# Optimization experiments

Hardware: AMD Instinct MI355X
Metric: run time of the kernel (lower is better)

## Reference

```python
import jax, jax.numpy as jnp
import numpy as np

D = 33        # n_vertices
HID = 256     # hidden_features
N_RANKS = 5


def setup_inputs() -> dict:
    key = jax.random.key(0)
    ks = jax.random.split(key, 8)
    img = jax.random.uniform(ks[0], (1, 3, 2160, 3840), dtype=jnp.float32)
    param = jax.random.normal(ks[1], (1, N_RANKS), dtype=jnp.float32) * 0.1

    def lin(k, fan_in, fan_out):
        lim = 1.0 / np.sqrt(fan_in)
        kw, kb = jax.random.split(k)
        W = jax.random.uniform(kw, (fan_in, fan_out), minval=-lim, maxval=lim, dtype=jnp.float32)
        b = jax.random.uniform(kb, (fan_out,), minval=-lim, maxval=lim, dtype=jnp.float32)
        return W, b

    W0, b0 = lin(ks[2], 11, HID)
    W1, b1 = lin(ks[3], HID, HID)
    W2, b2 = lin(ks[4], HID, HID)
    W3, b3 = lin(ks[5], HID, HID)
    W4, b4 = lin(ks[6], HID, 3)
    return dict(img=img, param=param, W0=W0, b0=b0, W1=W1, b1=b1,
                W2=W2, b2=b2, W3=W3, b3=b3, W4=W4, b4=b4)


def _identity_lut_flat():
    # torch: stack(meshgrid(ij), 0)/ (D-1), flip(0), reshape (1,3,D^3)
    v = jnp.arange(D, dtype=jnp.float32)
    g = jnp.stack(jnp.meshgrid(v, v, v, indexing='ij'), axis=0) / (D - 1)
    return g[::-1].reshape(1, 3, -1)  # (1, 3, 35937)


def _nilut(intensity, W0, b0, W1, b1, W2, b2, W3, b3, W4, b4):
    # intensity: (B, N, 8) = [r, g, b, params...]
    inp = jnp.concatenate([intensity, jnp.sort(intensity[..., :3], axis=-1)], axis=-1)  # (B,N,11)
    zero_inp = inp[:1].at[:, :, 3:-3].set(0.0)  # zero the param channels

    def net(x):
        h = jax.nn.relu(x @ W0 + b0)
        h = jnp.tanh(h @ W1 + b1)
        h = jnp.tanh(h @ W2 + b2)
        h = jnp.tanh(h @ W3 + b3)
        return h @ W4 + b4

    return net(inp) - net(zero_inp) + intensity[..., :3]


def _trilinear_lookup(img, luts):
    # img: (B,3,H,W) in [0,1]; luts: (B,3,D,D,D) indexed [c, b_idx, g_idx, r_idx]
    s = img * (D - 1)
    idx = jnp.clip(jnp.floor(s), 0, D - 2).astype(jnp.int32)
    f = s - idx.astype(s.dtype)

    def one(lut_b, idx_b, f_b):
        ir, ig, ib = idx_b[0], idx_b[1], idx_b[2]
        fr, fg, fb = f_b[0], f_b[1], f_b[2]

        def g(db, dg, dr):
            return lut_b[:, ib + db, ig + dg, ir + dr]  # (3,H,W)

        return (g(0, 0, 0) * (1 - fb) * (1 - fg) * (1 - fr)
                + g(0, 0, 1) * (1 - fb) * (1 - fg) * fr
                + g(0, 1, 0) * (1 - fb) * fg * (1 - fr)
                + g(0, 1, 1) * (1 - fb) * fg * fr
                + g(1, 0, 0) * fb * (1 - fg) * (1 - fr)
                + g(1, 0, 1) * fb * (1 - fg) * fr
                + g(1, 1, 0) * fb * fg * (1 - fr)
                + g(1, 1, 1) * fb * fg * fr)

    return jax.vmap(one)(luts, idx, f)


def reference(img, param, W0, b0, W1, b1, W2, b2, W3, b3, W4, b4):
    B = param.shape[0]
    ident = _identity_lut_flat()                              # (1,3,N)
    Nl = ident.shape[2]
    tiled = jnp.broadcast_to(param[:, :, None], (B, N_RANKS, Nl))
    ins = jnp.concatenate([jnp.broadcast_to(ident, (B, 3, Nl)), tiled], axis=1)  # (B,8,N)
    ins = jnp.transpose(ins, (0, 2, 1))                       # (B,N,8)
    luts = _nilut(ins, W0, b0, W1, b1, W2, b2, W3, b3, W4, b4)  # (B,N,3)
    luts = jnp.transpose(luts, (0, 2, 1)).reshape(B, 3, D, D, D)
    img_rep = jnp.broadcast_to(img, (B,) + img.shape[1:])
    return _trilinear_lookup(img_rep, luts)
```

## Files before the change

### kernel.cpp

```cpp
#include <hip/hip_runtime.h>
#include <hip/hip_fp16.h>
#include <math.h>

#define NPTS 35937
#define HID 256
#define TPB 256

typedef __attribute__((ext_vector_type(8))) short short8;
typedef __attribute__((ext_vector_type(4))) float f32x4;

__device__ __forceinline__ float fast_tanh(float x) {
    float e = __expf(2.0f * x);
    return 1.0f - __fdividef(2.0f, e + 1.0f);
}

__device__ __forceinline__ short f2bf(float f) {
    union { float f; unsigned u; } v; v.f = f;
    unsigned r = (v.u + 0x7fffu + ((v.u >> 16) & 1u)) >> 16;
    return (short)r;
}

__device__ __forceinline__ unsigned cvt_pk_bf16(float a, float b) {
    unsigned r;
    asm("v_cvt_pk_bf16_f32 %0, %1, %2" : "=v"(r) : "v"(a), "v"(b));
    return r;
}

#define W1P_OFF 8192
#define W2P_OFF 73728
#define W3P_OFF 139264
#define W4P_OFF 204800
#define CELL_BYTE_OFF 992896

__global__ __launch_bounds__(256) void pack_weights_kernel(
    const float* __restrict__ W0, const float* __restrict__ W1,
    const float* __restrict__ W2, const float* __restrict__ W3,
    const float* __restrict__ W4, short* __restrict__ P)
{
    int id = blockIdx.x * 256 + threadIdx.x;
    if (id >= 26112) return;
    const float* W; int f, NT, KREAL, NROW; long pbase;
    if (id < 1024)       { W = W0; f = id;         NT = 16; KREAL = 11;  NROW = 256; pbase = 0; }
    else if (id < 9216)  { W = W1; f = id - 1024;  NT = 16; KREAL = 256; NROW = 256; pbase = W1P_OFF; }
    else if (id < 17408) { W = W2; f = id - 9216;  NT = 16; KREAL = 256; NROW = 256; pbase = W2P_OFF; }
    else if (id < 25600) { W = W3; f = id - 17408; NT = 16; KREAL = 256; NROW = 256; pbase = W3P_OFF; }
    else                 { W = W4; f = id - 25600; NT = 1;  KREAL = 256; NROW = 3;   pbase = W4P_OFF; }
    int lane = f & 63;
    int tile = f >> 6;
    int nt = tile % NT, kt = tile / NT;
    int n  = nt * 16 + (lane & 15);
    int k0 = kt * 32 + ((lane >> 4) & 3) * 8;
    short v[8];
    #pragma unroll
    for (int j = 0; j < 8; ++j) {
        int k = k0 + j;
        float x = (k < KREAL && n < NROW) ? W[k * NROW + n] : 0.0f;
        v[j] = f2bf(x);
    }
    *(short8*)(P + pbase + (long)f * 8) = *(short8*)v;
}

#define HSTR 264

__global__ __launch_bounds__(256) void nilut_mfma_kernel(
    const float* __restrict__ param, const short* __restrict__ P,
    const float* __restrict__ b0, const float* __restrict__ b1,
    const float* __restrict__ b2, const float* __restrict__ b3,
    const float* __restrict__ b4, __half* __restrict__ cells)
{
    __shared__ short Hs[32][HSTR];
    __shared__ short Is[32][40];
    __shared__ float OB[32][4];

    const int t = threadIdx.x;
    const int pblock = blockIdx.x * 16;
    const int lane = t & 63;
    const int wid  = t >> 6;
    const int lr = lane & 15;
    const int hi = lane >> 4;
    const int k8 = hi * 8;

    if (t < 32) {
        int pn = pblock + (t >> 1);
        if (pn >= NPTS) pn = NPTS - 1;
        int v = t & 1;
        int ii = pn / 1089;
        int rem = pn - ii * 1089;
        int jj = rem / 33;
        int kk = rem - jj * 33;
        float r = kk * (1.0f / 32.0f);
        float g = jj * (1.0f / 32.0f);
        float b = ii * (1.0f / 32.0f);
        float lo = fminf(r, fminf(g, b));
        float hv = fmaxf(r, fmaxf(g, b));
        float mid = r + g + b - lo - hv;
        Is[t][0] = f2bf(r); Is[t][1] = f2bf(g); Is[t][2] = f2bf(b);
        #pragma unroll
        for (int q = 0; q < 5; ++q)
            Is[t][3 + q] = (v == 0) ? f2bf(param[q]) : (short)0;
        Is[t][8] = f2bf(lo); Is[t][9] = f2bf(mid); Is[t][10] = f2bf(hv);
        #pragma unroll
        for (int q = 11; q < 40; ++q) Is[t][q] = (short)0;
    }
    __syncthreads();

    f32x4 acc[2][4];
    const int nbase = wid * 64 + hi * 4;

    {
        #pragma unroll
        for (int c = 0; c < 4; ++c) {
            float4 bv = *(const float4*)(b0 + nbase + c * 16);
            f32x4 in = {bv.x, bv.y, bv.z, bv.w};
            #pragma unroll
            for (int rt = 0; rt < 2; ++rt) acc[rt][c] = in;
        }
        short8 a[2], bfr[4];
        #pragma unroll
        for (int rt = 0; rt < 2; ++rt) a[rt] = *(const short8*)&Is[rt * 16 + lr][k8];
        #pragma unroll
        for (int c = 0; c < 4; ++c)
            bfr[c] = *(const short8*)(P + ((long)(wid * 4 + c) * 64 + lane) * 8);
        #pragma unroll
        for (int rt = 0; rt < 2; ++rt)
            #pragma unroll
            for (int c = 0; c < 4; ++c)
                acc[rt][c] = __builtin_amdgcn_mfma_f32_16x16x32_bf16(bfr[c], a[rt], acc[rt][c], 0, 0, 0);
        #pragma unroll
        for (int rt = 0; rt < 2; ++rt)
            #pragma unroll
            for (int c = 0; c < 4; ++c) {
                uint2 w;
                w.x = cvt_pk_bf16(fmaxf(acc[rt][c][0], 0.0f), fmaxf(acc[rt][c][1], 0.0f));
                w.y = cvt_pk_bf16(fmaxf(acc[rt][c][2], 0.0f), fmaxf(acc[rt][c][3], 0.0f));
                *(uint2*)&Hs[rt * 16 + lr][nbase + c * 16] = w;
            }
    }
    __syncthreads();

    const long loff[3] = {W1P_OFF, W2P_OFF, W3P_OFF};
    const float* bptr[3];
    bptr[0] = b1; bptr[1] = b2; bptr[2] = b3;
    for (int L = 0; L < 3; ++L) {
        const short* WL = P + loff[L];
        const float* bb = bptr[L];
        #pragma unroll
        for (int c = 0; c < 4; ++c) {
            float4 bv = *(const float4*)(bb + nbase + c * 16);
            f32x4 in = {bv.x, bv.y, bv.z, bv.w};
            #pragma unroll
            for (int rt = 0; rt < 2; ++rt) acc[rt][c] = in;
        }
        #pragma unroll
        for (int kt = 0; kt < 8; ++kt) {
            short8 a[2], bfr[4];
            #pragma unroll
            for (int rt = 0; rt < 2; ++rt)
                a[rt] = *(const short8*)&Hs[rt * 16 + lr][kt * 32 + k8];
            #pragma unroll
            for (int c = 0; c < 4; ++c)
                bfr[c] = *(const short8*)(WL + ((long)(kt * 16 + wid * 4 + c) * 64 + lane) * 8);
            #pragma unroll
            for (int rt = 0; rt < 2; ++rt)
                #pragma unroll
                for (int c = 0; c < 4; ++c)
                    acc[rt][c] = __builtin_amdgcn_mfma_f32_16x16x32_bf16(bfr[c], a[rt], acc[rt][c], 0, 0, 0);
        }
        __syncthreads();
        #pragma unroll
        for (int rt = 0; rt < 2; ++rt)
            #pragma unroll
            for (int c = 0; c < 4; ++c) {
                uint2 w;
                w.x = cvt_pk_bf16(fast_tanh(acc[rt][c][0]), fast_tanh(acc[rt][c][1]));
                w.y = cvt_pk_bf16(fast_tanh(acc[rt][c][2]), fast_tanh(acc[rt][c][3]));
                *(uint2*)&Hs[rt * 16 + lr][nbase + c * 16] = w;
            }
        __syncthreads();
    }

    if (wid < 2) {
        float bv = (lr < 3) ? b4[lr] : 0.0f;
        f32x4 a4 = {bv, bv, bv, bv};
        const short* WL = P + W4P_OFF;
        #pragma unroll
        for (int kt = 0; kt < 8; ++kt) {
            short8 a = *(const short8*)&Hs[wid * 16 + lr][kt * 32 + k8];
            short8 b = *(const short8*)(WL + ((long)kt * 64 + lane) * 8);
            a4 = __builtin_amdgcn_mfma_f32_16x16x32_bf16(a, b, a4, 0, 0, 0);
        }
        if (lr < 3) {
            #pragma unroll
            for (int q = 0; q < 4; ++q)
                OB[wid * 16 + hi * 4 + q][lr] = a4[q];
        }
    }
    __syncthreads();

    if (t < 16) {
        int n = pblock + t;
        if (n < NPTS) {
            int ii = n / 1089;
            int rem = n - ii * 1089;
            int jj = rem / 33;
            int kk = rem - jj * 33;
            float vr = OB[2 * t][0] - OB[2 * t + 1][0] + kk * (1.0f / 32.0f);
            float vg = OB[2 * t][1] - OB[2 * t + 1][1] + jj * (1.0f / 32.0f);
            float vb = OB[2 * t][2] - OB[2 * t + 1][2] + ii * (1.0f / 32.0f);
            union { __half h[4]; uint2 u; } pk;
            pk.h[0] = __float2half_rn(vr);
            pk.h[1] = __float2half_rn(vg);
            pk.h[2] = __float2half_rn(vb);
            pk.h[3] = __float2half_rn(0.0f);
            #pragma unroll
            for (int corner = 0; corner < 8; ++corner) {
                int dr = corner & 1, dg = (corner >> 1) & 1, db = corner >> 2;
                int cr = kk - dr, cg = jj - dg, cb = ii - db;
                if ((unsigned)cr < 32u && (unsigned)cg < 32u && (unsigned)cb < 32u) {
                    long cell = cb * 1024 + cg * 32 + cr;
                    *(uint2*)(cells + cell * 32 + corner * 4) = pk.u;
                }
            }
        }
    }
}

#define LERP(a, b, f) fmaf((f), (b) - (a), (a))

__global__ __launch_bounds__(256) void apply_lut_kernel(
    const float* __restrict__ img, const __half* __restrict__ cells,
    float* __restrict__ out)
{
    const int NP = 2160 * 3840;
    int idx = blockIdx.x * blockDim.x + threadIdx.x;
    int p = idx * 4;
    if (p >= NP) return;

    float4 rv = *(const float4*)(img + p);
    float4 gv = *(const float4*)(img + NP + p);
    float4 bv = *(const float4*)(img + 2 * NP + p);

    float rr[4] = {rv.x, rv.y, rv.z, rv.w};
    float gg[4] = {gv.x, gv.y, gv.z, gv.w};
    float bb[4] = {bv.x, bv.y, bv.z, bv.w};
    float ox[4], oy[4], oz[4];

    #pragma unroll
    for (int u = 0; u < 4; ++u) {
        float sr = rr[u] * 32.0f, sg = gg[u] * 32.0f, sb = bb[u] * 32.0f;
        float fir = fminf(fmaxf(floorf(sr), 0.0f), 31.0f);
        float fig = fminf(fmaxf(floorf(sg), 0.0f), 31.0f);
        float fib = fminf(fmaxf(floorf(sb), 0.0f), 31.0f);
        float fr = sr - fir, fg = sg - fig, fb = sb - fib;
        int ir = (int)fir, ig = (int)fig, ib = (int)fib;

        const short8* cb = (const short8*)(cells + ((long)(ib * 1024 + ig * 32 + ir)) * 32);
        union { short8 s; __half h[8]; } u0, u1, u2, u3;
        u0.s = cb[0]; u1.s = cb[1]; u2.s = cb[2]; u3.s = cb[3];

        float v00[3], v01[3], v10[3], v11[3];
        #pragma unroll
        for (int c = 0; c < 3; ++c) {
            v00[c] = LERP(__half2float(u0.h[c]), __half2float(u0.h[c + 4]), fr);
            v01[c] = LERP(__half2float(u1.h[c]), __half2float(u1.h[c + 4]), fr);
            v10[c] = LERP(__half2float(u2.h[c]), __half2float(u2.h[c + 4]), fr);
            v11[c] = LERP(__half2float(u3.h[c]), __half2float(u3.h[c + 4]), fr);
        }
        ox[u] = LERP(LERP(v00[0], v01[0], fg), LERP(v10[0], v11[0], fg), fb);
        oy[u] = LERP(LERP(v00[1], v01[1], fg), LERP(v10[1], v11[1], fg), fb);
        oz[u] = LERP(LERP(v00[2], v01[2], fg), LERP(v10[2], v11[2], fg), fb);
    }

    *(float4*)(out + p)          = make_float4(ox[0], ox[1], ox[2], ox[3]);
    *(float4*)(out + NP + p)     = make_float4(oy[0], oy[1], oy[2], oy[3]);
    *(float4*)(out + 2 * NP + p) = make_float4(oz[0], oz[1], oz[2], oz[3]);
}

extern "C" void kernel_launch(void* const* d_in, const int* in_sizes, int n_in,
                              void* d_out, int out_size, void* d_ws, size_t ws_size,
                              hipStream_t stream) {
    const float* img   = (const float*)d_in[0];
    const float* param = (const float*)d_in[1];
    const float* W0 = (const float*)d_in[2];
    const float* b0 = (const float*)d_in[3];
    const float* W1 = (const float*)d_in[4];
    const float* b1 = (const float*)d_in[5];
    const float* W2 = (const float*)d_in[6];
    const float* b2 = (const float*)d_in[7];
    const float* W3 = (const float*)d_in[8];
    const float* b3 = (const float*)d_in[9];
    const float* W4 = (const float*)d_in[10];
    const float* b4 = (const float*)d_in[11];

    short*  P     = (short*)d_ws;
    __half* cells = (__half*)((char*)d_ws + CELL_BYTE_OFF);
    float*  out   = (float*)d_out;

    hipLaunchKernelGGL(pack_weights_kernel, dim3(102), dim3(TPB), 0, stream,
                       W0, W1, W2, W3, W4, P);

    int lut_blocks = (NPTS + 15) / 16;
    hipLaunchKernelGGL(nilut_mfma_kernel, dim3(lut_blocks), dim3(TPB), 0, stream,
                       param, P, b0, b1, b2, b3, b4, cells);

    const int NP = 2160 * 3840;
    int apply_blocks = (NP / 4 + TPB - 1) / TPB;
    hipLaunchKernelGGL(apply_lut_kernel, dim3(apply_blocks), dim3(TPB), 0, stream,
                       img, cells, out);
}
```

Before: 132.6 us.

## Double-buffer image tiles into LDS via async global_load_lds in apply kernel

```diff
diff --git a/kernel.cpp b/kernel.cpp
--- a/kernel.cpp
+++ b/kernel.cpp
@@ -226,54 +226,84 @@
 }
 
 #define LERP(a, b, f) fmaf((f), (b) - (a), (a))
+#define NP_TOTAL (2160 * 3840)
+#define AP_BLOCKS 2025
+#define AP_TILES 4
 
 __global__ __launch_bounds__(256) void apply_lut_kernel(
     const float* __restrict__ img, const __half* __restrict__ cells,
     float* __restrict__ out)
 {
-    const int NP = 2160 * 3840;
-    int idx = blockIdx.x * blockDim.x + threadIdx.x;
-    int p = idx * 4;
-    if (p >= NP) return;
-
-    float4 rv = *(const float4*)(img + p);
-    float4 gv = *(const float4*)(img + NP + p);
-    float4 bv = *(const float4*)(img + 2 * NP + p);
-
-    float rr[4] = {rv.x, rv.y, rv.z, rv.w};
-    float gg[4] = {gv.x, gv.y, gv.z, gv.w};
-    float bb[4] = {bv.x, bv.y, bv.z, bv.w};
-    float ox[4], oy[4], oz[4];
-
-    #pragma unroll
-    for (int u = 0; u < 4; ++u) {
-        float sr = rr[u] * 32.0f, sg = gg[u] * 32.0f, sb = bb[u] * 32.0f;
-        float fir = fminf(fmaxf(floorf(sr), 0.0f), 31.0f);
-        float fig = fminf(fmaxf(floorf(sg), 0.0f), 31.0f);
-        float fib = fminf(fmaxf(floorf(sb), 0.0f), 31.0f);
-        float fr = sr - fir, fg = sg - fig, fb = sb - fib;
-        int ir = (int)fir, ig = (int)fig, ib = (int)fib;
-
-        const short8* cb = (const short8*)(cells + ((long)(ib * 1024 + ig * 32 + ir)) * 32);
-        union { short8 s; __half h[8]; } u0, u1, u2, u3;
-        u0.s = cb[0]; u1.s = cb[1]; u2.s = cb[2]; u3.s = cb[3];
-
-        float v00[3], v01[3], v10[3], v11[3];
-        #pragma unroll
-        for (int c = 0; c < 3; ++c) {
-            v00[c] = LERP(__half2float(u0.h[c]), __half2float(u0.h[c + 4]), fr);
-            v01[c] = LERP(__half2float(u1.h[c]), __half2float(u1.h[c + 4]), fr);
-            v10[c] = LERP(__half2float(u2.h[c]), __half2float(u2.h[c + 4]), fr);
-            v11[c] = LERP(__half2float(u3.h[c]), __half2float(u3.h[c + 4]), fr);
-        }
-        ox[u] = LERP(LERP(v00[0], v01[0], fg), LERP(v10[0], v11[0], fg), fb);
-        oy[u] = LERP(LERP(v00[1], v01[1], fg), LERP(v10[1], v11[1], fg), fb);
-        oz[u] = LERP(LERP(v00[2], v01[2], fg), LERP(v10[2], v11[2], fg), fb);
-    }
-
-    *(float4*)(out + p)          = make_float4(ox[0], ox[1], ox[2], ox[3]);
-    *(float4*)(out + NP + p)     = make_float4(oy[0], oy[1], oy[2], oy[3]);
-    *(float4*)(out + 2 * NP + p) = make_float4(oz[0], oz[1], oz[2], oz[3]);
+    __shared__ float4 sbuf[2][3][256];
+
+    const int NP = NP_TOTAL;
+    const int tid = threadIdx.x;
+    const int w = tid >> 6;
+    const int lane = tid & 63;
+
+    {
+        long q0 = (long)(blockIdx.x * AP_TILES) * 256 + w * 64 + lane;
+        #pragma unroll
+        for (int pl = 0; pl < 3; ++pl)
+            __builtin_amdgcn_global_load_lds(
+                (const __attribute__((address_space(1))) void*)(img + (long)pl * NP + q0 * 4),
+                (__attribute__((address_space(3))) void*)&sbuf[0][pl][w * 64],
+                16, 0, 0);
+    }
+
+    for (int k = 0; k < AP_TILES; ++k) {
+        __syncthreads();
+
+        if (k + 1 < AP_TILES) {
+            long qn = (long)(blockIdx.x * AP_TILES + k + 1) * 256 + w * 64 + lane;
+            #pragma unroll
+            for (int pl = 0; pl < 3; ++pl)
+                __builtin_amdgcn_global_load_lds(
+                    (const __attribute__((address_space(1))) void*)(img + (long)pl * NP + qn * 4),
+                    (__attribute__((address_space(3))) void*)&sbuf[(k + 1) & 1][pl][w * 64],
+                    16, 0, 0);
+        }
+
+        float4 rv = sbuf[k & 1][0][tid];
+        float4 gv = sbuf[k & 1][1][tid];
+        float4 bv = sbuf[k & 1][2][tid];
+
+        float rr[4] = {rv.x, rv.y, rv.z, rv.w};
+        float gg[4] = {gv.x, gv.y, gv.z, gv.w};
+        float bb[4] = {bv.x, bv.y, bv.z, bv.w};
+        float ox[4], oy[4], oz[4];
+
+        #pragma unroll
+        for (int u = 0; u < 4; ++u) {
+            float sr = rr[u] * 32.0f, sg = gg[u] * 32.0f, sb = bb[u] * 32.0f;
+            float fir = fminf(fmaxf(floorf(sr), 0.0f), 31.0f);
+            float fig = fminf(fmaxf(floorf(sg), 0.0f), 31.0f);
+            float fib = fminf(fmaxf(floorf(sb), 0.0f), 31.0f);
+            float fr = sr - fir, fg = sg - fig, fb = sb - fib;
+            int ir = (int)fir, ig = (int)fig, ib = (int)fib;
+
+            const short8* cb = (const short8*)(cells + ((long)(ib * 1024 + ig * 32 + ir)) * 32);
+            union { short8 s; __half h[8]; } u0, u1, u2, u3;
+            u0.s = cb[0]; u1.s = cb[1]; u2.s = cb[2]; u3.s = cb[3];
+
+            float v00[3], v01[3], v10[3], v11[3];
+            #pragma unroll
+            for (int c = 0; c < 3; ++c) {
+                v00[c] = LERP(__half2float(u0.h[c]), __half2float(u0.h[c + 4]), fr);
+                v01[c] = LERP(__half2float(u1.h[c]), __half2float(u1.h[c + 4]), fr);
+                v10[c] = LERP(__half2float(u2.h[c]), __half2float(u2.h[c + 4]), fr);
+                v11[c] = LERP(__half2float(u3.h[c]), __half2float(u3.h[c + 4]), fr);
+            }
+            ox[u] = LERP(LERP(v00[0], v01[0], fg), LERP(v10[0], v11[0], fg), fb);
+            oy[u] = LERP(LERP(v00[1], v01[1], fg), LERP(v10[1], v11[1], fg), fb);
+            oz[u] = LERP(LERP(v00[2], v01[2], fg), LERP(v10[2], v11[2], fg), fb);
+        }
+
+        int p = (blockIdx.x * AP_TILES + k) * 1024 + tid * 4;
+        *(float4*)(out + p)          = make_float4(ox[0], ox[1], ox[2], ox[3]);
+        *(float4*)(out + NP + p)     = make_float4(oy[0], oy[1], oy[2], oy[3]);
+        *(float4*)(out + 2 * NP + p) = make_float4(oz[0], oz[1], oz[2], oz[3]);
+    }
 }
 
 extern "C" void kernel_launch(void* const* d_in, const int* in_sizes, int n_in,
@@ -303,8 +333,6 @@
     hipLaunchKernelGGL(nilut_mfma_kernel, dim3(lut_blocks), dim3(TPB), 0, stream,
                        param, P, b0, b1, b2, b3, b4, cells);
 
-    const int NP = 2160 * 3840;
-    int apply_blocks = (NP / 4 + TPB - 1) / TPB;
-    hipLaunchKernelGGL(apply_lut_kernel, dim3(apply_blocks), dim3(TPB), 0, stream,
+    hipLaunchKernelGGL(apply_lut_kernel, dim3(AP_BLOCKS), dim3(TPB), 0, stream,
                        img, cells, out);
 }
```

Measured after the change: 144.0 us. +8.7%, slower.
